# Kernel optimization log

Measured on AMD Instinct MI355X. Metric: run time of the kernel, lower is better.

The kernel has to match this reference:

```python
import jax, jax.numpy as jnp
import numpy as np

D = 1024      # d_model
H = 16        # num_heads
DK = D // H   # head dim = 64
C = 64        # chunk_size
MRP = 2 * C   # max_rel_pos = 128
B, S = 2, 2048


def setup_inputs() -> dict:
    key = jax.random.key(0)
    ks = jax.random.split(key, 7)
    s = 0.02
    x = jax.random.normal(ks[0], (B, S, D), jnp.float32)
    Wq = jax.random.normal(ks[1], (D, D), jnp.float32) * s
    Wk = jax.random.normal(ks[2], (D, D), jnp.float32) * s
    Wv = jax.random.normal(ks[3], (D, D), jnp.float32) * s
    Wo = jax.random.normal(ks[4], (D, D), jnp.float32) * s
    bq = jnp.zeros((D,), jnp.float32)
    bk = jnp.zeros((D,), jnp.float32)
    bv = jnp.zeros((D,), jnp.float32)
    bo = jnp.zeros((D,), jnp.float32)
    # torch init is zeros; use small values so the bias path is exercised
    rel_bias = jax.random.normal(ks[5], (2 * MRP + 1, H), jnp.float32) * s
    return dict(x=x, Wq=Wq, bq=bq, Wk=Wk, bk=bk, Wv=Wv, bv=bv, Wo=Wo, bo=bo,
                rel_bias=rel_bias)


def reference(x, Wq, bq, Wk, bk, Wv, bv, Wo, bo, rel_bias):
    b, s, _ = x.shape

    def heads(w, bias):
        return (x @ w + bias).reshape(b, s, H, DK).transpose(0, 2, 1, 3)  # [B,H,S,dk]

    Q = heads(Wq, bq)
    K = heads(Wk, bk)
    V = heads(Wv, bv)

    scale = jnp.sqrt(jnp.asarray(DK, x.dtype))
    scores = jnp.einsum('bhqd,bhkd->bhqk', Q, K) / scale  # [B,H,S,S]

    pos = jnp.arange(s)
    # chunked path's rel index reduces to global (q - k), clamped
    rel = jnp.clip(pos[:, None] - pos[None, :], -MRP, MRP) + MRP  # [S,S]
    bias2 = rel_bias[rel].transpose(2, 0, 1)  # [H,S,S]
    scores = scores + bias2[None]

    # growing-window chunk mask: query chunk i sees key chunks 0..i
    qc = pos // C
    allowed = qc[None, :] <= qc[:, None]  # [S_q, S_k]
    scores = jnp.where(allowed[None, None], scores, -jnp.inf)

    attn = jax.nn.softmax(scores, axis=-1)
    out = jnp.einsum('bhqk,bhkd->bhqd', attn, V)
    out = out.transpose(0, 2, 1, 3).reshape(b, s, D)
    return out @ Wo + bo
```

## Files before the change

### kernel.cpp

```cpp
#include <hip/hip_runtime.h>
#include <stdint.h>

#define NH 16
#define DKH 64
#define SEQ 2048
#define NBATCH 2
#define NROW (NBATCH*SEQ)
#define DM 1024
#define LOG2E 1.44269504088896f

typedef __attribute__((ext_vector_type(8))) __bf16 bf16x8;
typedef __attribute__((ext_vector_type(4))) float f32x4;

__device__ __forceinline__ unsigned short f2bf(float f) {
  union { float f; uint32_t u; } v; v.f = f;
  uint32_t r = v.u + 0x7FFFu + ((v.u >> 16) & 1u);
  return (unsigned short)(r >> 16);
}
__device__ __forceinline__ float bf2f(unsigned short b) {
  union { uint32_t u; float f; } v; v.u = ((uint32_t)b) << 16;
  return v.f;
}
__device__ __forceinline__ f32x4 mfma16(bf16x8 a, bf16x8 b, f32x4 c) {
  return __builtin_amdgcn_mfma_f32_16x16x32_bf16(a, b, c, 0, 0, 0);
}
__device__ __forceinline__ void gload_lds16(const void* g, void* l) {
  __builtin_amdgcn_global_load_lds(
      (__attribute__((address_space(1))) uint32_t*)(uintptr_t)g,
      (__attribute__((address_space(3))) uint32_t*)(uintptr_t)l,
      16, 0, 0);
}

__global__ __launch_bounds__(256) void k_cvt_x(const float* __restrict__ x,
                                               unsigned short* __restrict__ xb) {
  int i = blockIdx.x * 256 + threadIdx.x;
  float4 v = ((const float4*)x)[i];
  ushort4 o;
  o.x = f2bf(v.x); o.y = f2bf(v.y); o.z = f2bf(v.z); o.w = f2bf(v.w);
  ((ushort4*)xb)[i] = o;
}

__global__ __launch_bounds__(256) void k_cvt_w(
    const float* __restrict__ Wq, const float* __restrict__ Wk,
    const float* __restrict__ Wv, const float* __restrict__ Wo,
    unsigned short* __restrict__ Wqt, unsigned short* __restrict__ Wkt,
    unsigned short* __restrict__ Wvt, unsigned short* __restrict__ Wot) {
  __shared__ float tile[32][33];
  int z = blockIdx.z;
  const float* W = (z == 0) ? Wq : (z == 1) ? Wk : (z == 2) ? Wv : Wo;
  int ti = blockIdx.x, tj = blockIdx.y;
  int c = threadIdx.x & 31, r0 = threadIdx.x >> 5;
#pragma unroll
  for (int rr = 0; rr < 4; ++rr) {
    int r = r0 + rr * 8;
    tile[r][c] = W[(ti * 32 + r) * DM + tj * 32 + c];
  }
  __syncthreads();
  unsigned short* Out = (z == 0) ? Wqt : (z == 1) ? Wkt : (z == 2) ? Wvt : Wot;
#pragma unroll
  for (int rr = 0; rr < 4; ++rr) {
    int a = r0 + rr * 8;
    float v = tile[c][a];
    Out[(tj * 32 + a) * DM + ti * 32 + c] = f2bf(v);
  }
}

__global__ __launch_bounds__(256) void k_gemm_qkv(
    const unsigned short* __restrict__ xb,
    const unsigned short* __restrict__ Wqt, const unsigned short* __restrict__ Wkt,
    const unsigned short* __restrict__ Wvt,
    const float* __restrict__ bq, const float* __restrict__ bk,
    const float* __restrict__ bv,
    unsigned short* __restrict__ Q, unsigned short* __restrict__ Ko,
    unsigned short* __restrict__ Vt) {
  __shared__ __align__(16) unsigned short Al[128 * 64];
  __shared__ __align__(16) unsigned short Bl[128 * 64];
  int z = blockIdx.z;
  const unsigned short* Wt = (z == 0) ? Wqt : (z == 1) ? Wkt : Wvt;
  const float* bias = (z == 0) ? bq : (z == 1) ? bk : bv;

  int m0 = blockIdx.x * 128, n0 = blockIdx.y * 128;
  int tid = threadIdx.x, lane = tid & 63, wave = tid >> 6;
  int wr = wave >> 1, wc = wave & 1;
  int l15 = lane & 15, lg = lane >> 4;
  int r3 = lane >> 3, s3 = lane & 7;
  int gsw = (s3 ^ r3) << 4;
  int swz = l15 & 7;

  f32x4 acc[4][4] = {};

  for (int kb = 0; kb < 16; ++kb) {
#pragma unroll
    for (int c = 0; c < 4; ++c) {
      int rb = c * 32 + wave * 8;
      gload_lds16((const char*)xb + (size_t)(m0 + rb + r3) * 2048 + kb * 128 + gsw,
                  (char*)Al + rb * 128);
      gload_lds16((const char*)Wt + (size_t)(n0 + rb + r3) * 2048 + kb * 128 + gsw,
                  (char*)Bl + rb * 128);
    }
    __syncthreads();
#pragma unroll
    for (int ks = 0; ks < 2; ++ks) {
      int slot = lg + 4 * ks;
      int sofs = ((slot ^ swz) << 4);
      bf16x8 a[4], b[4];
#pragma unroll
      for (int mt = 0; mt < 4; ++mt)
        a[mt] = *(const bf16x8*)((const char*)Al + (wr * 64 + mt * 16 + l15) * 128 + sofs);
#pragma unroll
      for (int nt = 0; nt < 4; ++nt)
        b[nt] = *(const bf16x8*)((const char*)Bl + (wc * 64 + nt * 16 + l15) * 128 + sofs);
#pragma unroll
      for (int mt = 0; mt < 4; ++mt)
#pragma unroll
        for (int nt = 0; nt < 4; ++nt)
          acc[mt][nt] = mfma16(a[mt], b[nt], acc[mt][nt]);
    }
    __syncthreads();
  }

#pragma unroll
  for (int nt = 0; nt < 4; ++nt) {
    int n = n0 + wc * 64 + nt * 16 + l15;
    float bb = bias[n];
    int h = n >> 6, dk = n & 63;
#pragma unroll
    for (int mt = 0; mt < 4; ++mt) {
      int mbase = m0 + wr * 64 + mt * 16 + lg * 4;
      int bidx = mbase >> 11, s = mbase & 2047;
      if (z < 2) {
        unsigned short* Out = (z == 0) ? Q : Ko;
#pragma unroll
        for (int r = 0; r < 4; ++r)
          Out[(((size_t)(bidx * NH + h)) * SEQ + s + r) * DKH + dk] =
              f2bf(acc[mt][nt][r] + bb);
      } else {
        ushort4 pk;
        pk.x = f2bf(acc[mt][nt][0] + bb);
        pk.y = f2bf(acc[mt][nt][1] + bb);
        pk.z = f2bf(acc[mt][nt][2] + bb);
        pk.w = f2bf(acc[mt][nt][3] + bb);
        *(ushort4*)&Vt[((size_t)(bidx * NH + h) * DKH + dk) * SEQ + s] = pk;
      }
    }
  }
}

__global__ __launch_bounds__(256) void k_attn(
    const unsigned short* __restrict__ Qg, const unsigned short* __restrict__ Kg,
    const unsigned short* __restrict__ Vtg, const float* __restrict__ rel_bias,
    unsigned short* __restrict__ AOh) {
  __shared__ __align__(16) unsigned short Kl[2][64 * 64];
  __shared__ __align__(16) unsigned short Vl[2][64 * 64];
  __shared__ __align__(16) unsigned short Pl[64 * 72];
  __shared__ float biasl[257];

  int blk = blockIdx.x;
  int bh = blk & 31;
  int qc = 31 - (blk >> 5);
  int h = bh & 15, bidx = bh >> 4;
  int tid = threadIdx.x, lane = tid & 63, wave = tid >> 6;
  int l15 = lane & 15, lg = lane >> 4;
  int r3 = lane >> 3, s3 = lane & 7;
  int gsw = (s3 ^ r3) * 16;

  const float C1L = 0.125f * LOG2E;

  for (int i = tid; i < 257; i += 256)
    biasl[i] = rel_bias[i * NH + h] * LOG2E - 6.0f * LOG2E;

  int qrow = qc * 64 + wave * 16 + l15;
  const unsigned short* qptr = Qg + ((size_t)bh * SEQ + qrow) * DKH + lg * 8;
  bf16x8 qf0 = *(const bf16x8*)(qptr);
  bf16x8 qf1 = *(const bf16x8*)(qptr + 32);

  const char* kcb = (const char*)(Kg + (size_t)bh * SEQ * DKH);
  const char* vcb = (const char*)(Vtg + (size_t)bh * DKH * SEQ);

  auto stage = [&](int j, int b) {
    const char* kj = kcb + (size_t)j * (64 * DKH * 2);
    const char* vj = vcb + (size_t)j * 128;
#pragma unroll
    for (int c = 0; c < 2; ++c) {
      int rb = wave * 16 + c * 8;
      gload_lds16(kj + (size_t)(rb + r3) * 128 + gsw,
                  (char*)&Kl[b][0] + rb * 128);
      gload_lds16(vj + (size_t)(rb + r3) * (SEQ * 2) + gsw,
                  (char*)&Vl[b][0] + rb * 128);
    }
  };

  float lsum[4] = {0.f, 0.f, 0.f, 0.f};
  f32x4 acc[4] = {};

  stage(0, 0);
  asm volatile("s_waitcnt vmcnt(0)" ::: "memory");
  __syncthreads();
  float cfar = biasl[256];
  int swz = (l15 & 7);

  for (int j = 0; j <= qc; ++j) {
    int cur = j & 1;
    if (j < qc) stage(j + 1, cur ^ 1);

    const char* Kc = (const char*)&Kl[cur][0];
    const char* Vc = (const char*)&Vl[cur][0];

    f32x4 sa[4] = {};
#pragma unroll
    for (int ks = 0; ks < 2; ++ks) {
      bf16x8 qa = ks ? qf1 : qf0;
      int slot = lg + 4 * ks;
#pragma unroll
      for (int kt = 0; kt < 4; ++kt) {
        bf16x8 bb = *(const bf16x8*)(Kc + (kt * 16 + l15) * 128 + ((slot ^ swz) * 16));
        sa[kt] = mfma16(qa, bb, sa[kt]);
      }
    }

    float p[4][4];
    if (j >= qc - 2) {
      int kgb = j * 64 + l15;
      int qgb = qc * 64 + wave * 16 + lg * 4;
#pragma unroll
      for (int kt = 0; kt < 4; ++kt)
#pragma unroll
        for (int r = 0; r < 4; ++r) {
          int rel = (qgb + r) - (kgb + kt * 16);
          rel = min(max(rel, -128), 128) + 128;
          p[kt][r] = exp2f(fmaf(sa[kt][r], C1L, biasl[rel]));
        }
    } else {
#pragma unroll
      for (int kt = 0; kt < 4; ++kt)
#pragma unroll
        for (int r = 0; r < 4; ++r)
          p[kt][r] = exp2f(fmaf(sa[kt][r], C1L, cfar));
    }
#pragma unroll
    for (int r = 0; r < 4; ++r)
      lsum[r] += (p[0][r] + p[1][r]) + (p[2][r] + p[3][r]);

#pragma unroll
    for (int kt = 0; kt < 4; ++kt)
#pragma unroll
      for (int r = 0; r < 4; ++r) {
        __bf16 pb = (__bf16)p[kt][r];
        Pl[(wave * 16 + lg * 4 + r) * 72 + kt * 16 + l15] = *(unsigned short*)&pb;
      }

#pragma unroll
    for (int ks = 0; ks < 2; ++ks) {
      bf16x8 pa = *(const bf16x8*)((const char*)Pl +
                    (wave * 16 + l15) * 144 + lg * 16 + ks * 64);
      int slot = lg + 4 * ks;
#pragma unroll
      for (int dt = 0; dt < 4; ++dt) {
        bf16x8 vb = *(const bf16x8*)(Vc + (dt * 16 + l15) * 128 + ((slot ^ swz) * 16));
        acc[dt] = mfma16(pa, vb, acc[dt]);
      }
    }

    asm volatile("s_waitcnt vmcnt(0)" ::: "memory");
    __syncthreads();
  }

#pragma unroll
  for (int r = 0; r < 4; ++r) {
    float s = lsum[r];
#pragma unroll
    for (int off = 1; off < 16; off <<= 1) s += __shfl_xor(s, off);
    lsum[r] = s;
  }

#pragma unroll
  for (int r = 0; r < 4; ++r) {
    float inv = 1.0f / lsum[r];
    int s = qc * 64 + wave * 16 + lg * 4 + r;
    size_t row = (size_t)bidx * SEQ + s;
#pragma unroll
    for (int dt = 0; dt < 4; ++dt) {
      float v = acc[dt][r] * inv;
      int col = h * 64 + dt * 16 + l15;
      AOh[row * DM + col] = f2bf(v);
    }
  }
}

__global__ __launch_bounds__(256) void k_gemm_out(
    const unsigned short* __restrict__ Ab, const unsigned short* __restrict__ Bt,
    const float* __restrict__ bo, float* __restrict__ out) {
  __shared__ __align__(16) unsigned short Al[128 * 64];
  __shared__ __align__(16) unsigned short Bl[128 * 64];

  int m0 = blockIdx.x * 128, n0 = blockIdx.y * 128;
  int tid = threadIdx.x, lane = tid & 63, wave = tid >> 6;
  int wr = wave >> 1, wc = wave & 1;
  int l15 = lane & 15, lg = lane >> 4;
  int r3 = lane >> 3, s3 = lane & 7;
  int gsw = (s3 ^ r3) << 4;
  int swz = l15 & 7;

  f32x4 acc[4][4] = {};

  for (int kb = 0; kb < 16; ++kb) {
#pragma unroll
    for (int c = 0; c < 4; ++c) {
      int rb = c * 32 + wave * 8;
      gload_lds16((const char*)Ab + (size_t)(m0 + rb + r3) * 2048 + kb * 128 + gsw,
                  (char*)Al + rb * 128);
      gload_lds16((const char*)Bt + (size_t)(n0 + rb + r3) * 2048 + kb * 128 + gsw,
                  (char*)Bl + rb * 128);
    }
    __syncthreads();
#pragma unroll
    for (int ks = 0; ks < 2; ++ks) {
      int slot = lg + 4 * ks;
      int sofs = ((slot ^ swz) << 4);
      bf16x8 a[4], b[4];
#pragma unroll
      for (int mt = 0; mt < 4; ++mt)
        a[mt] = *(const bf16x8*)((const char*)Al + (wr * 64 + mt * 16 + l15) * 128 + sofs);
#pragma unroll
      for (int nt = 0; nt < 4; ++nt)
        b[nt] = *(const bf16x8*)((const char*)Bl + (wc * 64 + nt * 16 + l15) * 128 + sofs);
#pragma unroll
      for (int mt = 0; mt < 4; ++mt)
#pragma unroll
        for (int nt = 0; nt < 4; ++nt)
          acc[mt][nt] = mfma16(a[mt], b[nt], acc[mt][nt]);
    }
    __syncthreads();
  }

#pragma unroll
  for (int nt = 0; nt < 4; ++nt) {
    int n = n0 + wc * 64 + nt * 16 + l15;
    float bb = bo[n];
#pragma unroll
    for (int mt = 0; mt < 4; ++mt) {
      int mbase = m0 + wr * 64 + mt * 16 + lg * 4;
#pragma unroll
      for (int r = 0; r < 4; ++r)
        out[(size_t)(mbase + r) * DM + n] = acc[mt][nt][r] + bb;
    }
  }
}

extern "C" void kernel_launch(void* const* d_in, const int* in_sizes, int n_in,
                              void* d_out, int out_size, void* d_ws, size_t ws_size,
                              hipStream_t stream) {
  const float* x  = (const float*)d_in[0];
  const float* Wq = (const float*)d_in[1];
  const float* bq = (const float*)d_in[2];
  const float* Wk = (const float*)d_in[3];
  const float* bk = (const float*)d_in[4];
  const float* Wv = (const float*)d_in[5];
  const float* bv = (const float*)d_in[6];
  const float* Wo = (const float*)d_in[7];
  const float* bo = (const float*)d_in[8];
  const float* rb = (const float*)d_in[9];
  float* out = (float*)d_out;

  char* ws = (char*)d_ws;
  size_t off = 0;
  auto alloc = [&](size_t bytes) {
    char* p = ws + off; off += (bytes + 255) & ~(size_t)255; return p;
  };
  unsigned short* xb   = (unsigned short*)alloc((size_t)NROW * DM * 2);
  unsigned short* Wqt  = (unsigned short*)alloc((size_t)DM * DM * 2);
  unsigned short* Wkt  = (unsigned short*)alloc((size_t)DM * DM * 2);
  unsigned short* Wvt  = (unsigned short*)alloc((size_t)DM * DM * 2);
  unsigned short* Wot  = (unsigned short*)alloc((size_t)DM * DM * 2);
  unsigned short* Qb   = (unsigned short*)alloc((size_t)NROW * DM * 2);
  unsigned short* Kb   = (unsigned short*)alloc((size_t)NROW * DM * 2);
  unsigned short* Vtb  = (unsigned short*)alloc((size_t)NROW * DM * 2);
  unsigned short* AOh  = (unsigned short*)alloc((size_t)NROW * DM * 2);

  k_cvt_x<<<dim3(NROW * DM / 4 / 256), dim3(256), 0, stream>>>(x, xb);
  k_cvt_w<<<dim3(32, 32, 4), dim3(256), 0, stream>>>(Wq, Wk, Wv, Wo,
                                                     Wqt, Wkt, Wvt, Wot);
  k_gemm_qkv<<<dim3(32, 8, 3), dim3(256), 0, stream>>>(xb, Wqt, Wkt, Wvt,
                                                       bq, bk, bv, Qb, Kb, Vtb);
  k_attn<<<dim3(1024), dim3(256), 0, stream>>>(Qb, Kb, Vtb, rb, AOh);
  k_gemm_out<<<dim3(32, 8), dim3(256), 0, stream>>>(AOh, Wot, bo, out);
}
```

Before: 123.5 us.

## Double-buffer GEMM LDS staging and transpose score MFMA in attention

The QKV and output projection GEMMs now use two LDS buffers, prefetch two k-blocks ahead and use partial vmcnt waits with raw barriers, so global loads overlap MFMA work. The attention kernel swaps the MFMA operand order so each lane holds scores for one query row. That turns the P store into packed 4-element writes and the row sum into a single scalar with two shuffles. It also drops explicit vmcnt waits before the barriers, which relies on __syncthreads covering async LDS loads and risks a race if it does not.

```diff
diff --git a/kernel.cpp b/kernel.cpp
--- a/kernel.cpp
+++ b/kernel.cpp
@@ -10,16 +10,13 @@
 #define LOG2E 1.44269504088896f
 
 typedef __attribute__((ext_vector_type(8))) __bf16 bf16x8;
+typedef __attribute__((ext_vector_type(4))) __bf16 bf16x4;
 typedef __attribute__((ext_vector_type(4))) float f32x4;
 
 __device__ __forceinline__ unsigned short f2bf(float f) {
   union { float f; uint32_t u; } v; v.f = f;
   uint32_t r = v.u + 0x7FFFu + ((v.u >> 16) & 1u);
   return (unsigned short)(r >> 16);
-}
-__device__ __forceinline__ float bf2f(unsigned short b) {
-  union { uint32_t u; float f; } v; v.u = ((uint32_t)b) << 16;
-  return v.f;
 }
 __device__ __forceinline__ f32x4 mfma16(bf16x8 a, bf16x8 b, f32x4 c) {
   return __builtin_amdgcn_mfma_f32_16x16x32_bf16(a, b, c, 0, 0, 0);
@@ -29,6 +26,11 @@
       (__attribute__((address_space(1))) uint32_t*)(uintptr_t)g,
       (__attribute__((address_space(3))) uint32_t*)(uintptr_t)l,
       16, 0, 0);
+}
+__device__ __forceinline__ void barrier_raw() {
+  asm volatile("" ::: "memory");
+  __builtin_amdgcn_s_barrier();
+  asm volatile("" ::: "memory");
 }
 
 __global__ __launch_bounds__(256) void k_cvt_x(const float* __restrict__ x,
@@ -73,8 +75,8 @@
     const float* __restrict__ bv,
     unsigned short* __restrict__ Q, unsigned short* __restrict__ Ko,
     unsigned short* __restrict__ Vt) {
-  __shared__ __align__(16) unsigned short Al[128 * 64];
-  __shared__ __align__(16) unsigned short Bl[128 * 64];
+  __shared__ __align__(16) unsigned short Al[2][128 * 64];
+  __shared__ __align__(16) unsigned short Bl[2][128 * 64];
   int z = blockIdx.z;
   const unsigned short* Wt = (z == 0) ? Wqt : (z == 1) ? Wkt : Wvt;
   const float* bias = (z == 0) ? bq : (z == 1) ? bk : bv;
@@ -89,34 +91,44 @@
 
   f32x4 acc[4][4] = {};
 
-  for (int kb = 0; kb < 16; ++kb) {
+  auto stage = [&](int kb, int b) {
 #pragma unroll
     for (int c = 0; c < 4; ++c) {
       int rb = c * 32 + wave * 8;
       gload_lds16((const char*)xb + (size_t)(m0 + rb + r3) * 2048 + kb * 128 + gsw,
-                  (char*)Al + rb * 128);
+                  (char*)&Al[b][0] + rb * 128);
       gload_lds16((const char*)Wt + (size_t)(n0 + rb + r3) * 2048 + kb * 128 + gsw,
-                  (char*)Bl + rb * 128);
-    }
-    __syncthreads();
+                  (char*)&Bl[b][0] + rb * 128);
+    }
+  };
+
+  stage(0, 0);
+  stage(1, 1);
+
+  for (int kb = 0; kb < 16; ++kb) {
+    if (kb < 15) asm volatile("s_waitcnt vmcnt(8)" ::: "memory");
+    else         asm volatile("s_waitcnt vmcnt(0)" ::: "memory");
+    barrier_raw();
+    int b = kb & 1;
 #pragma unroll
     for (int ks = 0; ks < 2; ++ks) {
       int slot = lg + 4 * ks;
       int sofs = ((slot ^ swz) << 4);
-      bf16x8 a[4], b[4];
+      bf16x8 a[4], bfr[4];
 #pragma unroll
       for (int mt = 0; mt < 4; ++mt)
-        a[mt] = *(const bf16x8*)((const char*)Al + (wr * 64 + mt * 16 + l15) * 128 + sofs);
+        a[mt] = *(const bf16x8*)((const char*)&Al[b][0] + (wr * 64 + mt * 16 + l15) * 128 + sofs);
 #pragma unroll
       for (int nt = 0; nt < 4; ++nt)
-        b[nt] = *(const bf16x8*)((const char*)Bl + (wc * 64 + nt * 16 + l15) * 128 + sofs);
+        bfr[nt] = *(const bf16x8*)((const char*)&Bl[b][0] + (wc * 64 + nt * 16 + l15) * 128 + sofs);
 #pragma unroll
       for (int mt = 0; mt < 4; ++mt)
 #pragma unroll
         for (int nt = 0; nt < 4; ++nt)
-          acc[mt][nt] = mfma16(a[mt], b[nt], acc[mt][nt]);
-    }
-    __syncthreads();
+          acc[mt][nt] = mfma16(a[mt], bfr[nt], acc[mt][nt]);
+    }
+    barrier_raw();
+    if (kb < 14) stage(kb + 2, b);
   }
 
 #pragma unroll
@@ -190,11 +202,10 @@
     }
   };
 
-  float lsum[4] = {0.f, 0.f, 0.f, 0.f};
+  float lsum = 0.f;
   f32x4 acc[4] = {};
 
   stage(0, 0);
-  asm volatile("s_waitcnt vmcnt(0)" ::: "memory");
   __syncthreads();
   float cfar = biasl[256];
   int swz = (l15 & 7);
@@ -213,20 +224,19 @@
       int slot = lg + 4 * ks;
 #pragma unroll
       for (int kt = 0; kt < 4; ++kt) {
-        bf16x8 bb = *(const bf16x8*)(Kc + (kt * 16 + l15) * 128 + ((slot ^ swz) * 16));
-        sa[kt] = mfma16(qa, bb, sa[kt]);
+        bf16x8 kfr = *(const bf16x8*)(Kc + (kt * 16 + l15) * 128 + ((slot ^ swz) * 16));
+        sa[kt] = mfma16(kfr, qa, sa[kt]);
       }
     }
 
     float p[4][4];
     if (j >= qc - 2) {
-      int kgb = j * 64 + l15;
-      int qgb = qc * 64 + wave * 16 + lg * 4;
+      int kb0 = j * 64 + lg * 4;
 #pragma unroll
       for (int kt = 0; kt < 4; ++kt)
 #pragma unroll
         for (int r = 0; r < 4; ++r) {
-          int rel = (qgb + r) - (kgb + kt * 16);
+          int rel = qrow - (kb0 + kt * 16 + r);
           rel = min(max(rel, -128), 128) + 128;
           p[kt][r] = exp2f(fmaf(sa[kt][r], C1L, biasl[rel]));
         }
@@ -238,16 +248,16 @@
           p[kt][r] = exp2f(fmaf(sa[kt][r], C1L, cfar));
     }
 #pragma unroll
-    for (int r = 0; r < 4; ++r)
-      lsum[r] += (p[0][r] + p[1][r]) + (p[2][r] + p[3][r]);
-
-#pragma unroll
     for (int kt = 0; kt < 4; ++kt)
-#pragma unroll
-      for (int r = 0; r < 4; ++r) {
-        __bf16 pb = (__bf16)p[kt][r];
-        Pl[(wave * 16 + lg * 4 + r) * 72 + kt * 16 + l15] = *(unsigned short*)&pb;
-      }
+      lsum += (p[kt][0] + p[kt][1]) + (p[kt][2] + p[kt][3]);
+
+#pragma unroll
+    for (int kt = 0; kt < 4; ++kt) {
+      bf16x4 pk;
+      pk[0] = (__bf16)p[kt][0]; pk[1] = (__bf16)p[kt][1];
+      pk[2] = (__bf16)p[kt][2]; pk[3] = (__bf16)p[kt][3];
+      *(bf16x4*)&Pl[(wave * 16 + l15) * 72 + kt * 16 + lg * 4] = pk;
+    }
 
 #pragma unroll
     for (int ks = 0; ks < 2; ++ks) {
@@ -261,21 +271,15 @@
       }
     }
 
-    asm volatile("s_waitcnt vmcnt(0)" ::: "memory");
     __syncthreads();
   }
 
+  lsum += __shfl_xor(lsum, 16);
+  lsum += __shfl_xor(lsum, 32);
+
 #pragma unroll
   for (int r = 0; r < 4; ++r) {
-    float s = lsum[r];
-#pragma unroll
-    for (int off = 1; off < 16; off <<= 1) s += __shfl_xor(s, off);
-    lsum[r] = s;
-  }
-
-#pragma unroll
-  for (int r = 0; r < 4; ++r) {
-    float inv = 1.0f / lsum[r];
+    float inv = 1.0f / __shfl(lsum, lg * 4 + r, 64);
     int s = qc * 64 + wave * 16 + lg * 4 + r;
     size_t row = (size_t)bidx * SEQ + s;
 #pragma unroll
@@ -290,8 +294,8 @@
 __global__ __launch_bounds__(256) void k_gemm_out(
     const unsigned short* __restrict__ Ab, const unsigned short* __restrict__ Bt,
     const float* __restrict__ bo, float* __restrict__ out) {
-  __shared__ __align__(16) unsigned short Al[128 * 64];
-  __shared__ __align__(16) unsigned short Bl[128 * 64];
+  __shared__ __align__(16) unsigned short Al[2][128 * 64];
+  __shared__ __align__(16) unsigned short Bl[2][128 * 64];
 
   int m0 = blockIdx.x * 128, n0 = blockIdx.y * 128;
   int tid = threadIdx.x, lane = tid & 63, wave = tid >> 6;
@@ -303,34 +307,44 @@
 
   f32x4 acc[4][4] = {};
 
-  for (int kb = 0; kb < 16; ++kb) {
+  auto stage = [&](int kb, int b) {
 #pragma unroll
     for (int c = 0; c < 4; ++c) {
       int rb = c * 32 + wave * 8;
       gload_lds16((const char*)Ab + (size_t)(m0 + rb + r3) * 2048 + kb * 128 + gsw,
-                  (char*)Al + rb * 128);
+                  (char*)&Al[b][0] + rb * 128);
       gload_lds16((const char*)Bt + (size_t)(n0 + rb + r3) * 2048 + kb * 128 + gsw,
-                  (char*)Bl + rb * 128);
-    }
-    __syncthreads();
+                  (char*)&Bl[b][0] + rb * 128);
+    }
+  };
+
+  stage(0, 0);
+  stage(1, 1);
+
+  for (int kb = 0; kb < 16; ++kb) {
+    if (kb < 15) asm volatile("s_waitcnt vmcnt(8)" ::: "memory");
+    else         asm volatile("s_waitcnt vmcnt(0)" ::: "memory");
+    barrier_raw();
+    int b = kb & 1;
 #pragma unroll
     for (int ks = 0; ks < 2; ++ks) {
       int slot = lg + 4 * ks;
       int sofs = ((slot ^ swz) << 4);
-      bf16x8 a[4], b[4];
+      bf16x8 a[4], bfr[4];
 #pragma unroll
       for (int mt = 0; mt < 4; ++mt)
-        a[mt] = *(const bf16x8*)((const char*)Al + (wr * 64 + mt * 16 + l15) * 128 + sofs);
+        a[mt] = *(const bf16x8*)((const char*)&Al[b][0] + (wr * 64 + mt * 16 + l15) * 128 + sofs);
 #pragma unroll
       for (int nt = 0; nt < 4; ++nt)
-        b[nt] = *(const bf16x8*)((const char*)Bl + (wc * 64 + nt * 16 + l15) * 128 + sofs);
+        bfr[nt] = *(const bf16x8*)((const char*)&Bl[b][0] + (wc * 64 + nt * 16 + l15) * 128 + sofs);
 #pragma unroll
       for (int mt = 0; mt < 4; ++mt)
 #pragma unroll
         for (int nt = 0; nt < 4; ++nt)
-          acc[mt][nt] = mfma16(a[mt], b[nt], acc[mt][nt]);
-    }
-    __syncthreads();
+          acc[mt][nt] = mfma16(a[mt], bfr[nt], acc[mt][nt]);
+    }
+    barrier_raw();
+    if (kb < 14) stage(kb + 2, b);
   }
 
 #pragma unroll
```

New measurement: 107.1 us. -13.3%, faster.
